# Kernel tuning notes

Measured on AMD Instinct MI355X. Metric: run time of the kernel, lower is better.

The kernel has to match this reference:

```python
import jax, jax.numpy as jnp
import numpy as np

D = 1024      # d_model
B = 16        # batch size
L = 1024      # query length
NE = 20000    # global number of entities
NB = 256      # entities per batch element (with -1 padding)
N_PAD = 32    # padded (-1) entity slots per row


def setup_inputs() -> dict:
    key = jax.random.key(0)
    ks = jax.random.split(key, 10)
    s = 1.0 / np.sqrt(D)  # torch nn.Linear default init range
    query = jax.random.normal(ks[0], (B, L, D), jnp.float32)
    ent_emb = jax.random.normal(ks[1], (NE, D), jnp.float32)
    idx = jax.random.randint(ks[2], (B, NB), 0, NE)
    idx = idx.at[:, -N_PAD:].set(-1)  # padding entities -> masked out
    WQ_w = jax.random.uniform(ks[3], (D, D), jnp.float32, -s, s)
    WQ_b = jax.random.uniform(ks[4], (D,), jnp.float32, -s, s)
    WK_w = jax.random.uniform(ks[5], (D, D), jnp.float32, -s, s)
    WK_b = jax.random.uniform(ks[6], (D,), jnp.float32, -s, s)
    WO_w = jax.random.uniform(ks[7], (D, D), jnp.float32, -s, s)
    WO_b = jax.random.uniform(ks[8], (D,), jnp.float32, -s, s)
    ln_g = jnp.ones((D,), jnp.float32)
    ln_b = jnp.zeros((D,), jnp.float32)
    return dict(query=query, ent_emb=ent_emb, ent_idx_in_batch=idx,
                max_entity_number=512,
                WQ_w=WQ_w, WQ_b=WQ_b, WK_w=WK_w, WK_b=WK_b,
                WO_w=WO_w, WO_b=WO_b, ln_g=ln_g, ln_b=ln_b)


def reference(query, ent_emb, ent_idx_in_batch, max_entity_number,
              WQ_w, WQ_b, WK_w, WK_b, WO_w, WO_b, ln_g, ln_b):
    # mask: 1.0 for real entities, 0.0 for -1 padding. (B, NB, 1)
    mask = (ent_idx_in_batch != -1).astype(query.dtype)[:, :, None]
    # gather per-batch entity embeddings (negative index wraps, then masked)
    ent_g = ent_emb[ent_idx_in_batch]                    # (B, NB, D)
    q = query @ WQ_w.T + WQ_b                            # (B, L, D)
    ent = (ent_g @ WK_w.T + WK_b) * mask                 # (B, NB, D)
    # attention scores with additive mask, then softmax
    w = jnp.einsum('byd,bnd->byn', q, ent)               # (B, L, NB)
    w = w - (1.0 - mask[:, :, 0])[:, None, :] * 100000.0
    w = jax.nn.softmax(w, axis=-1)
    # NOTE: original code uses WK (not WV) for values, and scales AFTER softmax
    d_model = query.shape[-1]
    v = jnp.einsum('byn,bnd->byd', w * (float(d_model) ** -0.5), ent)
    v = v @ WO_w.T + WO_b                                # (B, L, D)
    mu = jnp.mean(v, axis=-1, keepdims=True)
    var = jnp.var(v, axis=-1, keepdims=True)             # biased, as torch LN
    v = (v - mu) / jnp.sqrt(var + 1e-5) * ln_g + ln_b
    return v
```

## Files before the change

kernel.cpp:

```cpp
#include <hip/hip_runtime.h>
#include <hip/hip_bf16.h>
#include <cstdint>
#include <cstddef>

typedef _Float16 f16;
typedef _Float16 f16x8 __attribute__((ext_vector_type(8)));
typedef _Float16 f16x4 __attribute__((ext_vector_type(4)));
typedef float    f32x4 __attribute__((ext_vector_type(4)));

#define DM 1024
#define NBE 256

__global__ __launch_bounds__(256) void prep(
    const float* __restrict__ WO_w, f16* __restrict__ WOr,
    const float* __restrict__ WQ_w, const float* __restrict__ WK_w,
    f16* __restrict__ WQt, f16* __restrict__ WKt,
    const float* __restrict__ ent_emb, const int* __restrict__ idx,
    f16* __restrict__ Egh,
    const float* __restrict__ WQ_b, const float* __restrict__ WK_b,
    float* __restrict__ u, float* __restrict__ wobk) {
  __shared__ float ts[64][65];
  __shared__ float sm4[4];
  int blk = blockIdx.x, tid = threadIdx.x;
  if (blk < 1024) {
    int i = (blk * 256 + tid) * 4;
    float4 v = *(const float4*)(WO_w + i);
    f16x4 o; o.x = (f16)v.x; o.y = (f16)v.y; o.z = (f16)v.z; o.w = (f16)v.w;
    *(f16x4*)(WOr + i) = o;
  } else if (blk < 1536) {
    int t = blk - 1024;
    const float* in = (t >> 8) ? WK_w : WQ_w;
    f16* out = (t >> 8) ? WKt : WQt;
    int bi = ((t >> 4) & 15) * 64, bj = (t & 15) * 64;
    int tx = tid & 63, ty = tid >> 6;
#pragma unroll
    for (int k = 0; k < 16; ++k) {
      int r = ty * 16 + k;
      ts[r][tx] = in[(size_t)(bi + r) * DM + bj + tx];
    }
    __syncthreads();
#pragma unroll
    for (int k = 0; k < 16; ++k) {
      int r = ty * 16 + k;
      out[(size_t)(bj + r) * DM + bi + tx] = (f16)ts[tx][r];
    }
  } else if (blk < 5632) {
    int slot = blk - 1536;
    int e = idx[slot];
    int c = tid * 4;
    f16x4 o;
    if (e < 0) {
      o.x = (f16)0.f; o.y = (f16)0.f; o.z = (f16)0.f; o.w = (f16)0.f;
    } else {
      float4 v = *(const float4*)(ent_emb + (size_t)e * DM + c);
      o.x = (f16)v.x; o.y = (f16)v.y; o.z = (f16)v.z; o.w = (f16)v.w;
    }
    *(f16x4*)(Egh + (size_t)slot * DM + c) = o;
  } else if (blk < 5637) {
    int t = blk - 5632;
    if (t < 4) {
      int k = t * 256 + tid;
      float s = 0.f;
      for (int d = 0; d < 1024; ++d) s += WQ_b[d] * WK_w[(size_t)d * 1024 + k];
      u[k] = s;
    } else {
      float s = 0.f;
      for (int i = tid; i < 1024; i += 256) s += WK_b[i] * WQ_b[i];
#pragma unroll
      for (int d = 1; d < 64; d <<= 1) s += __shfl_xor(s, d);
      int w = tid >> 6;
      if ((tid & 63) == 0) sm4[w] = s;
      __syncthreads();
      if (tid == 0) u[1024] = sm4[0] + sm4[1] + sm4[2] + sm4[3];
    }
  } else {
    int w = tid >> 6, lane = tid & 63;
    int r = (blk - 5637) * 4 + w;
    const float* a = WO_w + (size_t)r * 1024;
    float s = 0.f;
#pragma unroll
    for (int i = 0; i < 16; ++i) s += a[lane + i * 64] * WK_b[lane + i * 64];
#pragma unroll
    for (int d = 1; d < 64; d <<= 1) s += __shfl_xor(s, d);
    if (lane == 0) wobk[r] = s;
  }
}

template <int EPI>
__device__ __forceinline__ void gemm_core(
    const f16* __restrict__ A, const f16* __restrict__ B,
    const float* __restrict__ rowbias, const int* __restrict__ colidx,
    f16* __restrict__ C, int N, int K, int m0, int n0,
    f16* __restrict__ smA, f16* __restrict__ smB) {
  int tid = threadIdx.x;
  int lane = tid & 63, w = tid >> 6;
  int wr = w >> 1, wc = w & 1;
  int l15 = lane & 15, lhi = lane >> 4;
  const f16* Ab = A + (size_t)m0 * K;
  const f16* Bb = B + (size_t)n0 * K;

  f32x4 acc[4][4];
  f32x4 z4 = {0.f, 0.f, 0.f, 0.f};
#pragma unroll
  for (int i = 0; i < 4; ++i)
#pragma unroll
    for (int j = 0; j < 4; ++j) acc[i][j] = z4;

  f16x8 ra[4], rb[4];
#pragma unroll
  for (int p = 0; p < 4; ++p) {
    int e = p * 2048 + tid * 8;
    int row = e >> 6, c8 = (e & 63) >> 3;
    ra[p] = *(const f16x8*)(Ab + (size_t)row * K + c8 * 8);
    rb[p] = *(const f16x8*)(Bb + (size_t)row * K + c8 * 8);
  }
#pragma unroll
  for (int p = 0; p < 4; ++p) {
    int e = p * 2048 + tid * 8;
    int row = e >> 6, c8 = (e & 63) >> 3;
    int off = row * 64 + ((c8 ^ (row & 7)) << 3);
    *(f16x8*)(&smA[off]) = ra[p];
    *(f16x8*)(&smB[off]) = rb[p];
  }

  int nk = K >> 6;
  for (int kt = 0; kt < nk; ++kt) {
    int cur = kt & 1;
    bool pre = (kt + 1 < nk);
    __syncthreads();
    if (pre) {
      const f16* An = Ab + (kt + 1) * 64;
      const f16* Bn = Bb + (kt + 1) * 64;
#pragma unroll
      for (int p = 0; p < 4; ++p) {
        int e = p * 2048 + tid * 8;
        int row = e >> 6, c8 = (e & 63) >> 3;
        ra[p] = *(const f16x8*)(An + (size_t)row * K + c8 * 8);
        rb[p] = *(const f16x8*)(Bn + (size_t)row * K + c8 * 8);
      }
    }
    const f16* As = smA + cur * 8192;
    const f16* Bs = smB + cur * 8192;
    __builtin_amdgcn_s_setprio(1);
#pragma unroll
    for (int kk = 0; kk < 2; ++kk) {
      int c8 = kk * 4 + lhi;
      f16x8 af[4], bf[4];
#pragma unroll
      for (int mi = 0; mi < 4; ++mi) {
        int r = wr * 64 + mi * 16 + l15;
        af[mi] = *(const f16x8*)(As + r * 64 + ((c8 ^ (r & 7)) << 3));
      }
#pragma unroll
      for (int ni = 0; ni < 4; ++ni) {
        int r = wc * 64 + ni * 16 + l15;
        bf[ni] = *(const f16x8*)(Bs + r * 64 + ((c8 ^ (r & 7)) << 3));
      }
#pragma unroll
      for (int mi = 0; mi < 4; ++mi)
#pragma unroll
        for (int ni = 0; ni < 4; ++ni)
          acc[mi][ni] = __builtin_amdgcn_mfma_f32_16x16x32_f16(af[mi], bf[ni], acc[mi][ni], 0, 0, 0);
    }
    __builtin_amdgcn_s_setprio(0);
    if (pre) {
#pragma unroll
      for (int p = 0; p < 4; ++p) {
        int e = p * 2048 + tid * 8;
        int row = e >> 6, c8 = (e & 63) >> 3;
        int off = (cur ^ 1) * 8192 + row * 64 + ((c8 ^ (row & 7)) << 3);
        *(f16x8*)(&smA[off]) = ra[p];
        *(f16x8*)(&smB[off]) = rb[p];
      }
    }
  }

#pragma unroll
  for (int mi = 0; mi < 4; ++mi) {
#pragma unroll
    for (int j = 0; j < 4; ++j) {
      int r = m0 + wr * 64 + mi * 16 + lhi * 4 + j;
      float rbv = (EPI == 3) ? rowbias[r] : 0.f;
#pragma unroll
      for (int ni = 0; ni < 4; ++ni) {
        int cN = n0 + wc * 64 + ni * 16 + l15;
        float v = acc[mi][ni][j];
        if (EPI == 3) { v += rbv; if (colidx[cN] < 0) v = 0.f; }
        C[(size_t)r * N + cN] = (f16)v;
      }
    }
  }
}

__global__ __launch_bounds__(256) void gemm_dual(const f16* __restrict__ A0,
                                                 const f16* __restrict__ A1,
                                                 const f16* __restrict__ B,
                                                 f16* __restrict__ C0,
                                                 f16* __restrict__ C1, int N, int K) {
  __shared__ __align__(16) f16 sA[2 * 8192], sB[2 * 8192];
  const f16* A = blockIdx.z ? A1 : A0;
  f16* C = blockIdx.z ? C1 : C0;
  gemm_core<0>(A, B, nullptr, nullptr, C, N, K, blockIdx.y * 128, blockIdx.x * 128, sA, sB);
}

__global__ __launch_bounds__(256) void gemm_pair(
    const f16* __restrict__ Egh, const f16* __restrict__ G, const f16* __restrict__ H,
    const float* __restrict__ wobk, const int* __restrict__ idx,
    const float* __restrict__ u,
    f16* __restrict__ Tp, f16* __restrict__ EWot, float* __restrict__ cvec) {
  __shared__ __align__(16) f16 sA[2 * 8192], sB[2 * 8192];
  int blk = blockIdx.x;
  if (blk < 256) {
    gemm_core<0>(Egh, G, nullptr, nullptr, Tp, 1024, 1024, (blk >> 3) * 128, (blk & 7) * 128, sA, sB);
  } else if (blk < 512) {
    int t = blk - 256;
    gemm_core<3>(H, Egh, wobk, idx, EWot, 4096, 1024, (t >> 5) * 128, (t & 31) * 128, sA, sB);
  } else {
    int t = blk - 512;
    int w = threadIdx.x >> 6, lane = threadIdx.x & 63;
    int n = t * 4 + w;
    const f16* e = Egh + (size_t)n * 1024;
    float s = 0.f;
#pragma unroll
    for (int i = 0; i < 16; ++i) { int k = lane + i * 64; s += (float)e[k] * u[k]; }
#pragma unroll
    for (int d = 1; d < 64; d <<= 1) s += __shfl_xor(s, d);
    if (lane == 0)
      cvec[n] = s + u[1024] + ((idx[n] < 0) ? -100000.0f : 0.0f);
  }
}

__global__ __launch_bounds__(256, 2) void attn3(
    const float* __restrict__ query, const f16* __restrict__ Tp,
    const f16* __restrict__ EWot, const float* __restrict__ cvec,
    f16* __restrict__ O16) {
  __shared__ __align__(16) char pool[49152];
  f16* smB = (f16*)pool;
  f16* smP = (f16*)(pool + 32768);
  f16* smQ = (f16*)(pool + 32768);
  __shared__ float smMax[64], smSum[64];
  int id = blockIdx.x;
  int b = id & 15, lt = id >> 4;
  int tid = threadIdx.x, lane = tid & 63, w = tid >> 6;
  int l15 = lane & 15, lhi = lane >> 4;
  int wq = w >> 1, wc = w & 1;
  const float* Qb = query + (size_t)(b * 1024 + lt * 32) * DM;
  const f16* Tb = Tp + (size_t)b * NBE * DM;

  f32x4 z4 = {0.f, 0.f, 0.f, 0.f};
  f32x4 accs[8];
#pragma unroll
  for (int i = 0; i < 8; ++i) accs[i] = z4;

  float4 rqa, rqb;
  f16x8 rb[8];
  int qrow = tid >> 3, qc0 = (tid & 7) * 8;

  rqa = *(const float4*)(Qb + (size_t)qrow * DM + qc0);
  rqb = *(const float4*)(Qb + (size_t)qrow * DM + qc0 + 4);
#pragma unroll
  for (int p = 0; p < 8; ++p) {
    int e = p * 2048 + tid * 8;
    int row = e >> 6, c8 = (e & 63) >> 3;
    rb[p] = *(const f16x8*)(Tb + (size_t)row * DM + c8 * 8);
  }

  for (int kt = 0; kt < 16; ++kt) {
    __syncthreads();
    {
      f16x8 h;
      h[0] = (f16)rqa.x; h[1] = (f16)rqa.y; h[2] = (f16)rqa.z; h[3] = (f16)rqa.w;
      h[4] = (f16)rqb.x; h[5] = (f16)rqb.y; h[6] = (f16)rqb.z; h[7] = (f16)rqb.w;
      int c8 = qc0 >> 3;
      *(f16x8*)(smQ + qrow * 64 + ((c8 ^ (qrow & 7)) << 3)) = h;
    }
#pragma unroll
    for (int p = 0; p < 8; ++p) {
      int e = p * 2048 + tid * 8;
      int row = e >> 6, c8 = (e & 63) >> 3;
      *(f16x8*)(smB + row * 64 + ((c8 ^ (row & 7)) << 3)) = rb[p];
    }
    __syncthreads();
    if (kt < 15) {
      rqa = *(const float4*)(Qb + (size_t)qrow * DM + (kt + 1) * 64 + qc0);
      rqb = *(const float4*)(Qb + (size_t)qrow * DM + (kt + 1) * 64 + qc0 + 4);
#pragma unroll
      for (int p = 0; p < 8; ++p) {
        int e = p * 2048 + tid * 8;
        int row = e >> 6, c8 = (e & 63) >> 3;
        rb[p] = *(const f16x8*)(Tb + (size_t)row * DM + (kt + 1) * 64 + c8 * 8);
      }
    }
    __builtin_amdgcn_s_setprio(1);
#pragma unroll
    for (int kk = 0; kk < 2; ++kk) {
      int c8 = kk * 4 + lhi;
      int qr = wq * 16 + l15;
      f16x8 aq = *(const f16x8*)(smQ + qr * 64 + ((c8 ^ (qr & 7)) << 3));
#pragma unroll
      for (int ni = 0; ni < 8; ++ni) {
        int er = wc * 128 + ni * 16 + l15;
        f16x8 bb = *(const f16x8*)(smB + er * 64 + ((c8 ^ (er & 7)) << 3));
        accs[ni] = __builtin_amdgcn_mfma_f32_16x16x32_f16(aq, bb, accs[ni], 0, 0, 0);
      }
    }
    __builtin_amdgcn_s_setprio(0);
  }

  const f16* Eb = EWot + (size_t)b * NBE;
#pragma unroll
  for (int p = 0; p < 8; ++p) {
    int e = p * 2048 + tid * 8;
    int row = e >> 6, c8 = (e & 63) >> 3;
    rb[p] = *(const f16x8*)(Eb + (size_t)row * 4096 + c8 * 8);
  }

  float cv[8];
#pragma unroll
  for (int ni = 0; ni < 8; ++ni)
    cv[ni] = cvec[b * NBE + wc * 128 + ni * 16 + l15];
  int rbase = wq * 16 + lhi * 4;
  float mxl[4], sml[4];
#pragma unroll
  for (int j = 0; j < 4; ++j) {
    float m = -3.0e38f;
#pragma unroll
    for (int ni = 0; ni < 8; ++ni) m = fmaxf(m, accs[ni][j] + cv[ni]);
    m = fmaxf(m, __shfl_xor(m, 1));
    m = fmaxf(m, __shfl_xor(m, 2));
    m = fmaxf(m, __shfl_xor(m, 4));
    m = fmaxf(m, __shfl_xor(m, 8));
    mxl[j] = m;
    if (l15 == 0) smMax[wc * 32 + rbase + j] = m;
  }
  __syncthreads();
#pragma unroll
  for (int j = 0; j < 4; ++j) {
    float fm = fmaxf(mxl[j], smMax[(wc ^ 1) * 32 + rbase + j]);
    float s = 0.f;
#pragma unroll
    for (int ni = 0; ni < 8; ++ni) {
      float e = __expf(accs[ni][j] + cv[ni] - fm);
      accs[ni][j] = e;
      s += e;
    }
    s += __shfl_xor(s, 1);
    s += __shfl_xor(s, 2);
    s += __shfl_xor(s, 4);
    s += __shfl_xor(s, 8);
    sml[j] = s;
    if (l15 == 0) smSum[wc * 32 + rbase + j] = s;
  }
  __syncthreads();
#pragma unroll
  for (int j = 0; j < 4; ++j) {
    float inv = 0.03125f / (sml[j] + smSum[(wc ^ 1) * 32 + rbase + j]);
    int r = rbase + j;
#pragma unroll
    for (int ni = 0; ni < 8; ++ni) {
      int col = wc * 128 + ni * 16 + l15;
      int cc8 = col >> 3;
      smP[r * 256 + ((cc8 ^ (r & 7)) << 3) + (col & 7)] = (f16)(accs[ni][j] * inv);
    }
  }

  f16* Ob = O16 + (size_t)(b * 1024 + lt * 32) * DM;
  for (int dc = 0; dc < 4; ++dc) {
    f32x4 accv[8];
#pragma unroll
    for (int i = 0; i < 8; ++i) accv[i] = z4;
    for (int ks = 0; ks < 4; ++ks) {
      __syncthreads();
#pragma unroll
      for (int p = 0; p < 8; ++p) {
        int e = p * 2048 + tid * 8;
        int row = e >> 6, c8 = (e & 63) >> 3;
        *(f16x8*)(smB + row * 64 + ((c8 ^ (row & 7)) << 3)) = rb[p];
      }
      __syncthreads();
      int nxt = dc * 4 + ks + 1;
      if (nxt < 16) {
        int ndc = nxt >> 2, nks = nxt & 3;
#pragma unroll
        for (int p = 0; p < 8; ++p) {
          int e = p * 2048 + tid * 8;
          int row = e >> 6, c8 = (e & 63) >> 3;
          rb[p] = *(const f16x8*)(Eb + (size_t)(ndc * 256 + row) * 4096 + nks * 64 + c8 * 8);
        }
      }
      __builtin_amdgcn_s_setprio(1);
#pragma unroll
      for (int kk = 0; kk < 2; ++kk) {
        int pc8 = ks * 8 + kk * 4 + lhi;
        int qr = wq * 16 + l15;
        f16x8 ap = *(const f16x8*)(smP + qr * 256 + ((pc8 ^ (qr & 7)) << 3));
        int c8 = kk * 4 + lhi;
#pragma unroll
        for (int ni = 0; ni < 8; ++ni) {
          int er = wc * 128 + ni * 16 + l15;
          f16x8 bv = *(const f16x8*)(smB + er * 64 + ((c8 ^ (er & 7)) << 3));
          accv[ni] = __builtin_amdgcn_mfma_f32_16x16x32_f16(ap, bv, accv[ni], 0, 0, 0);
        }
      }
      __builtin_amdgcn_s_setprio(0);
    }
#pragma unroll
    for (int ni = 0; ni < 8; ++ni) {
#pragma unroll
      for (int j = 0; j < 4; ++j) {
        int r = wq * 16 + lhi * 4 + j;
        int col = dc * 256 + wc * 128 + ni * 16 + l15;
        Ob[(size_t)r * DM + col] = (f16)accv[ni][j];
      }
    }
  }
}

__global__ __launch_bounds__(256) void ln_f16(const f16* __restrict__ X,
                                              const float* __restrict__ bo,
                                              const float* __restrict__ g,
                                              const float* __restrict__ bta,
                                              float* __restrict__ out) {
  size_t row = blockIdx.x;
  const f16* x = X + row * DM;
  int tid = threadIdx.x;
  f16x4 h = *(const f16x4*)(x + tid * 4);
  float4 bo4 = *(const float4*)(bo + tid * 4);
  float4 v;
  v.x = (float)h[0] + bo4.x; v.y = (float)h[1] + bo4.y;
  v.z = (float)h[2] + bo4.z; v.w = (float)h[3] + bo4.w;
  float s = v.x + v.y + v.z + v.w;
  float q = v.x * v.x + v.y * v.y + v.z * v.z + v.w * v.w;
#pragma unroll
  for (int d = 1; d < 64; d <<= 1) { s += __shfl_xor(s, d); q += __shfl_xor(q, d); }
  __shared__ float ss[4], qq[4];
  int w = tid >> 6, lane = tid & 63;
  if (lane == 0) { ss[w] = s; qq[w] = q; }
  __syncthreads();
  s = ss[0] + ss[1] + ss[2] + ss[3];
  q = qq[0] + qq[1] + qq[2] + qq[3];
  float mu = s * (1.0f / DM);
  float var = q * (1.0f / DM) - mu * mu;
  float rs = rsqrtf(var + 1e-5f);
  float4 gg = *(const float4*)(g + tid * 4);
  float4 bb = *(const float4*)(bta + tid * 4);
  float4 o;
  o.x = (v.x - mu) * rs * gg.x + bb.x;
  o.y = (v.y - mu) * rs * gg.y + bb.y;
  o.z = (v.z - mu) * rs * gg.z + bb.z;
  o.w = (v.w - mu) * rs * gg.w + bb.w;
  *(float4*)(out + row * DM + tid * 4) = o;
}

extern "C" void kernel_launch(void* const* d_in, const int* in_sizes, int n_in,
                              void* d_out, int out_size, void* d_ws, size_t ws_size,
                              hipStream_t stream) {
  const float* query   = (const float*)d_in[0];
  const float* ent_emb = (const float*)d_in[1];
  const int*   idx     = (const int*)d_in[2];
  const float* WQ_w = (const float*)d_in[4];
  const float* WQ_b = (const float*)d_in[5];
  const float* WK_w = (const float*)d_in[6];
  const float* WK_b = (const float*)d_in[7];
  const float* WO_w = (const float*)d_in[8];
  const float* WO_b = (const float*)d_in[9];
  const float* ln_g = (const float*)d_in[10];
  const float* ln_b = (const float*)d_in[11];
  float* out = (float*)d_out;

  char* p = (char*)d_ws;
  f16* Egh  = (f16*)p;  p += (size_t)4096 * 1024 * 2;
  f16* WQt  = (f16*)p;  p += (size_t)1024 * 1024 * 2;
  f16* WKt  = (f16*)p;  p += (size_t)1024 * 1024 * 2;
  f16* WOr  = (f16*)p;  p += (size_t)1024 * 1024 * 2;
  f16* G    = (f16*)p;  p += (size_t)1024 * 1024 * 2;
  f16* H    = (f16*)p;  p += (size_t)1024 * 1024 * 2;
  f16* Tp   = (f16*)p;  p += (size_t)4096 * 1024 * 2;
  f16* EWot = (f16*)p;  p += (size_t)1024 * 4096 * 2;
  f16* O16  = (f16*)p;  p += (size_t)16384 * 1024 * 2;
  float* u    = (float*)p; p += 1025 * 4;
  float* wobk = (float*)p; p += 1024 * 4;
  float* cvec = (float*)p; p += 4096 * 4;

  prep<<<5893, 256, 0, stream>>>(WO_w, WOr, WQ_w, WK_w, WQt, WKt,
                                 ent_emb, idx, Egh, WQ_b, WK_b, u, wobk);
  gemm_dual<<<dim3(8, 8, 2), 256, 0, stream>>>(WQt, WOr, WKt, G, H, 1024, 1024);
  gemm_pair<<<1536, 256, 0, stream>>>(Egh, G, H, wobk, idx, u, Tp, EWot, cvec);
  attn3<<<512, 256, 0, stream>>>(query, Tp, EWot, cvec, O16);
  ln_f16<<<16384, 256, 0, stream>>>(O16, WO_b, ln_g, ln_b, out);
}
```

Baseline: 308.0 us.

## Fuse LayerNorm into attention kernel with 64-row tiles and double-buffered LDS

The attention kernel now handles 64 query rows per block instead of 32, so 256 blocks replace 512. Q/T and EWot tiles are double-buffered in LDS, which needs one barrier per k-step instead of two, and each wave now owns a 64x64 output tile. The output bias add, row statistics and LayerNorm are fused into the kernel, which removes the separate ln_f16 launch. The f16 intermediate is still written and then re-read from global memory for the final normalization. Separately, the u-vector reduction in prep is split across 16 blocks with atomicAdd plus a memset, replacing 4 long serial loops. The larger tile and launch bound of 1 lower occupancy, and with only 256 blocks part of the GPU may sit idle.

```diff
diff --git a/kernel.cpp b/kernel.cpp
--- a/kernel.cpp
+++ b/kernel.cpp
@@ -56,26 +56,33 @@
       o.x = (f16)v.x; o.y = (f16)v.y; o.z = (f16)v.z; o.w = (f16)v.w;
     }
     *(f16x4*)(Egh + (size_t)slot * DM + c) = o;
-  } else if (blk < 5637) {
-    int t = blk - 5632;
-    if (t < 4) {
-      int k = t * 256 + tid;
-      float s = 0.f;
-      for (int d = 0; d < 1024; ++d) s += WQ_b[d] * WK_w[(size_t)d * 1024 + k];
-      u[k] = s;
-    } else {
-      float s = 0.f;
-      for (int i = tid; i < 1024; i += 256) s += WK_b[i] * WQ_b[i];
-#pragma unroll
-      for (int d = 1; d < 64; d <<= 1) s += __shfl_xor(s, d);
-      int w = tid >> 6;
-      if ((tid & 63) == 0) sm4[w] = s;
-      __syncthreads();
-      if (tid == 0) u[1024] = sm4[0] + sm4[1] + sm4[2] + sm4[3];
-    }
+  } else if (blk < 5648) {
+    int d0 = (blk - 5632) * 64;
+    float a0 = 0.f, a1 = 0.f, a2 = 0.f, a3 = 0.f;
+    for (int d = 0; d < 64; ++d) {
+      float bq = WQ_b[d0 + d];
+      const float* row = WK_w + (size_t)(d0 + d) * 1024;
+      a0 += bq * row[tid];
+      a1 += bq * row[tid + 256];
+      a2 += bq * row[tid + 512];
+      a3 += bq * row[tid + 768];
+    }
+    atomicAdd(&u[tid], a0);
+    atomicAdd(&u[tid + 256], a1);
+    atomicAdd(&u[tid + 512], a2);
+    atomicAdd(&u[tid + 768], a3);
+  } else if (blk < 5649) {
+    float s = 0.f;
+    for (int i = tid; i < 1024; i += 256) s += WK_b[i] * WQ_b[i];
+#pragma unroll
+    for (int d = 1; d < 64; d <<= 1) s += __shfl_xor(s, d);
+    int w = tid >> 6;
+    if ((tid & 63) == 0) sm4[w] = s;
+    __syncthreads();
+    if (tid == 0) u[1024] = sm4[0] + sm4[1] + sm4[2] + sm4[3];
   } else {
     int w = tid >> 6, lane = tid & 63;
-    int r = (blk - 5637) * 4 + w;
+    int r = (blk - 5649) * 4 + w;
     const float* a = WO_w + (size_t)r * 1024;
     float s = 0.f;
 #pragma unroll
@@ -230,226 +237,296 @@
   }
 }
 
-__global__ __launch_bounds__(256, 2) void attn3(
+__global__ __launch_bounds__(256, 1) void attn4(
     const float* __restrict__ query, const f16* __restrict__ Tp,
     const f16* __restrict__ EWot, const float* __restrict__ cvec,
-    f16* __restrict__ O16) {
-  __shared__ __align__(16) char pool[49152];
-  f16* smB = (f16*)pool;
-  f16* smP = (f16*)(pool + 32768);
-  f16* smQ = (f16*)(pool + 32768);
-  __shared__ float smMax[64], smSum[64];
+    const float* __restrict__ bo, const float* __restrict__ ln_g,
+    const float* __restrict__ ln_b, f16* __restrict__ O16,
+    float* __restrict__ out) {
+  __shared__ __align__(16) f16 smB[2][256 * 64];
+  __shared__ __align__(16) f16 smQ[2][64 * 64];
+  __shared__ __align__(16) f16 smP[64 * 256];
+  __shared__ float smS[256], smS2[256];
   int id = blockIdx.x;
   int b = id & 15, lt = id >> 4;
   int tid = threadIdx.x, lane = tid & 63, w = tid >> 6;
   int l15 = lane & 15, lhi = lane >> 4;
-  int wq = w >> 1, wc = w & 1;
-  const float* Qb = query + (size_t)(b * 1024 + lt * 32) * DM;
+  const float* Qb = query + (size_t)(b * 1024 + lt * 64) * DM;
   const f16* Tb = Tp + (size_t)b * NBE * DM;
+  const f16* Eb = EWot + (size_t)b * NBE;
+  size_t baserow = (size_t)(b * 1024 + lt * 64);
 
   f32x4 z4 = {0.f, 0.f, 0.f, 0.f};
-  f32x4 accs[8];
-#pragma unroll
-  for (int i = 0; i < 8; ++i) accs[i] = z4;
-
-  float4 rqa, rqb;
+  f32x4 acc[4][4];
+#pragma unroll
+  for (int i = 0; i < 4; ++i)
+#pragma unroll
+    for (int j = 0; j < 4; ++j) acc[i][j] = z4;
+
+  float4 rq[4];
   f16x8 rb[8];
-  int qrow = tid >> 3, qc0 = (tid & 7) * 8;
-
-  rqa = *(const float4*)(Qb + (size_t)qrow * DM + qc0);
-  rqb = *(const float4*)(Qb + (size_t)qrow * DM + qc0 + 4);
+  int qrow = tid >> 2, qc0 = (tid & 3) * 16;
+  int srow = tid >> 3, sc8 = tid & 7;
+
+#pragma unroll
+  for (int q = 0; q < 4; ++q) rq[q] = *(const float4*)(Qb + (size_t)qrow * DM + qc0 + q * 4);
+#pragma unroll
+  for (int p = 0; p < 8; ++p)
+    rb[p] = *(const f16x8*)(Tb + (size_t)(p * 32 + srow) * DM + sc8 * 8);
+  {
+    f16x8 h0, h1;
+    h0[0] = (f16)rq[0].x; h0[1] = (f16)rq[0].y; h0[2] = (f16)rq[0].z; h0[3] = (f16)rq[0].w;
+    h0[4] = (f16)rq[1].x; h0[5] = (f16)rq[1].y; h0[6] = (f16)rq[1].z; h0[7] = (f16)rq[1].w;
+    h1[0] = (f16)rq[2].x; h1[1] = (f16)rq[2].y; h1[2] = (f16)rq[2].z; h1[3] = (f16)rq[2].w;
+    h1[4] = (f16)rq[3].x; h1[5] = (f16)rq[3].y; h1[6] = (f16)rq[3].z; h1[7] = (f16)rq[3].w;
+    int c8a = (tid & 3) * 2;
+    *(f16x8*)(&smQ[0][qrow * 64 + ((c8a ^ (qrow & 7)) << 3)]) = h0;
+    *(f16x8*)(&smQ[0][qrow * 64 + (((c8a + 1) ^ (qrow & 7)) << 3)]) = h1;
+  }
 #pragma unroll
   for (int p = 0; p < 8; ++p) {
-    int e = p * 2048 + tid * 8;
-    int row = e >> 6, c8 = (e & 63) >> 3;
-    rb[p] = *(const f16x8*)(Tb + (size_t)row * DM + c8 * 8);
-  }
+    int row = p * 32 + srow;
+    *(f16x8*)(&smB[0][row * 64 + ((sc8 ^ (row & 7)) << 3)]) = rb[p];
+  }
+#pragma unroll
+  for (int q = 0; q < 4; ++q) rq[q] = *(const float4*)(Qb + (size_t)qrow * DM + 64 + qc0 + q * 4);
+#pragma unroll
+  for (int p = 0; p < 8; ++p)
+    rb[p] = *(const f16x8*)(Tb + (size_t)(p * 32 + srow) * DM + 64 + sc8 * 8);
+  __syncthreads();
 
   for (int kt = 0; kt < 16; ++kt) {
-    __syncthreads();
-    {
-      f16x8 h;
-      h[0] = (f16)rqa.x; h[1] = (f16)rqa.y; h[2] = (f16)rqa.z; h[3] = (f16)rqa.w;
-      h[4] = (f16)rqb.x; h[5] = (f16)rqb.y; h[6] = (f16)rqb.z; h[7] = (f16)rqb.w;
-      int c8 = qc0 >> 3;
-      *(f16x8*)(smQ + qrow * 64 + ((c8 ^ (qrow & 7)) << 3)) = h;
-    }
-#pragma unroll
-    for (int p = 0; p < 8; ++p) {
-      int e = p * 2048 + tid * 8;
-      int row = e >> 6, c8 = (e & 63) >> 3;
-      *(f16x8*)(smB + row * 64 + ((c8 ^ (row & 7)) << 3)) = rb[p];
-    }
-    __syncthreads();
+    int cur = kt & 1;
     if (kt < 15) {
-      rqa = *(const float4*)(Qb + (size_t)qrow * DM + (kt + 1) * 64 + qc0);
-      rqb = *(const float4*)(Qb + (size_t)qrow * DM + (kt + 1) * 64 + qc0 + 4);
+      f16x8 h0, h1;
+      h0[0] = (f16)rq[0].x; h0[1] = (f16)rq[0].y; h0[2] = (f16)rq[0].z; h0[3] = (f16)rq[0].w;
+      h0[4] = (f16)rq[1].x; h0[5] = (f16)rq[1].y; h0[6] = (f16)rq[1].z; h0[7] = (f16)rq[1].w;
+      h1[0] = (f16)rq[2].x; h1[1] = (f16)rq[2].y; h1[2] = (f16)rq[2].z; h1[3] = (f16)rq[2].w;
+      h1[4] = (f16)rq[3].x; h1[5] = (f16)rq[3].y; h1[6] = (f16)rq[3].z; h1[7] = (f16)rq[3].w;
+      int c8a = (tid & 3) * 2;
+      *(f16x8*)(&smQ[cur ^ 1][qrow * 64 + ((c8a ^ (qrow & 7)) << 3)]) = h0;
+      *(f16x8*)(&smQ[cur ^ 1][qrow * 64 + (((c8a + 1) ^ (qrow & 7)) << 3)]) = h1;
 #pragma unroll
       for (int p = 0; p < 8; ++p) {
-        int e = p * 2048 + tid * 8;
-        int row = e >> 6, c8 = (e & 63) >> 3;
-        rb[p] = *(const f16x8*)(Tb + (size_t)row * DM + (kt + 1) * 64 + c8 * 8);
-      }
+        int row = p * 32 + srow;
+        *(f16x8*)(&smB[cur ^ 1][row * 64 + ((sc8 ^ (row & 7)) << 3)]) = rb[p];
+      }
+    }
+    if (kt < 14) {
+#pragma unroll
+      for (int q = 0; q < 4; ++q)
+        rq[q] = *(const float4*)(Qb + (size_t)qrow * DM + (kt + 2) * 64 + qc0 + q * 4);
+#pragma unroll
+      for (int p = 0; p < 8; ++p)
+        rb[p] = *(const f16x8*)(Tb + (size_t)(p * 32 + srow) * DM + (kt + 2) * 64 + sc8 * 8);
     }
     __builtin_amdgcn_s_setprio(1);
 #pragma unroll
     for (int kk = 0; kk < 2; ++kk) {
       int c8 = kk * 4 + lhi;
-      int qr = wq * 16 + l15;
-      f16x8 aq = *(const f16x8*)(smQ + qr * 64 + ((c8 ^ (qr & 7)) << 3));
-#pragma unroll
-      for (int ni = 0; ni < 8; ++ni) {
-        int er = wc * 128 + ni * 16 + l15;
-        f16x8 bb = *(const f16x8*)(smB + er * 64 + ((c8 ^ (er & 7)) << 3));
-        accs[ni] = __builtin_amdgcn_mfma_f32_16x16x32_f16(aq, bb, accs[ni], 0, 0, 0);
-      }
+      f16x8 af[4], bf[4];
+#pragma unroll
+      for (int mi = 0; mi < 4; ++mi) {
+        int r = mi * 16 + l15;
+        af[mi] = *(const f16x8*)(&smQ[cur][r * 64 + ((c8 ^ (r & 7)) << 3)]);
+      }
+#pragma unroll
+      for (int ni = 0; ni < 4; ++ni) {
+        int er = w * 64 + ni * 16 + l15;
+        bf[ni] = *(const f16x8*)(&smB[cur][er * 64 + ((c8 ^ (er & 7)) << 3)]);
+      }
+#pragma unroll
+      for (int mi = 0; mi < 4; ++mi)
+#pragma unroll
+        for (int ni = 0; ni < 4; ++ni)
+          acc[mi][ni] = __builtin_amdgcn_mfma_f32_16x16x32_f16(af[mi], bf[ni], acc[mi][ni], 0, 0, 0);
     }
     __builtin_amdgcn_s_setprio(0);
-  }
-
-  const f16* Eb = EWot + (size_t)b * NBE;
+    __syncthreads();
+  }
+
+#pragma unroll
+  for (int p = 0; p < 8; ++p)
+    rb[p] = *(const f16x8*)(Eb + (size_t)(p * 32 + srow) * 4096 + sc8 * 8);
+
+  float cv[4];
+#pragma unroll
+  for (int ni = 0; ni < 4; ++ni)
+    cv[ni] = cvec[b * NBE + w * 64 + ni * 16 + l15];
+#pragma unroll
+  for (int mi = 0; mi < 4; ++mi)
+#pragma unroll
+    for (int j = 0; j < 4; ++j) {
+      float m = -3.0e38f;
+#pragma unroll
+      for (int ni = 0; ni < 4; ++ni) m = fmaxf(m, acc[mi][ni][j] + cv[ni]);
+      m = fmaxf(m, __shfl_xor(m, 1));
+      m = fmaxf(m, __shfl_xor(m, 2));
+      m = fmaxf(m, __shfl_xor(m, 4));
+      m = fmaxf(m, __shfl_xor(m, 8));
+      if (l15 == 0) smS[w * 64 + mi * 16 + lhi * 4 + j] = m;
+    }
+  __syncthreads();
+#pragma unroll
+  for (int mi = 0; mi < 4; ++mi)
+#pragma unroll
+    for (int j = 0; j < 4; ++j) {
+      int r = mi * 16 + lhi * 4 + j;
+      float fm = fmaxf(fmaxf(smS[r], smS[64 + r]), fmaxf(smS[128 + r], smS[192 + r]));
+      float s = 0.f;
+#pragma unroll
+      for (int ni = 0; ni < 4; ++ni) {
+        float e = __expf(acc[mi][ni][j] + cv[ni] - fm);
+        acc[mi][ni][j] = e;
+        s += e;
+      }
+      s += __shfl_xor(s, 1);
+      s += __shfl_xor(s, 2);
+      s += __shfl_xor(s, 4);
+      s += __shfl_xor(s, 8);
+      if (l15 == 0) smS2[w * 64 + r] = s;
+    }
+  __syncthreads();
+#pragma unroll
+  for (int mi = 0; mi < 4; ++mi)
+#pragma unroll
+    for (int j = 0; j < 4; ++j) {
+      int r = mi * 16 + lhi * 4 + j;
+      float inv = 0.03125f / (smS2[r] + smS2[64 + r] + smS2[128 + r] + smS2[192 + r]);
+#pragma unroll
+      for (int ni = 0; ni < 4; ++ni) {
+        int col = w * 64 + ni * 16 + l15;
+        int cc8 = col >> 3;
+        smP[r * 256 + ((cc8 ^ (r & 7)) << 3) + (col & 7)] = (f16)(acc[mi][ni][j] * inv);
+      }
+    }
+
 #pragma unroll
   for (int p = 0; p < 8; ++p) {
-    int e = p * 2048 + tid * 8;
-    int row = e >> 6, c8 = (e & 63) >> 3;
-    rb[p] = *(const f16x8*)(Eb + (size_t)row * 4096 + c8 * 8);
-  }
-
-  float cv[8];
-#pragma unroll
-  for (int ni = 0; ni < 8; ++ni)
-    cv[ni] = cvec[b * NBE + wc * 128 + ni * 16 + l15];
-  int rbase = wq * 16 + lhi * 4;
-  float mxl[4], sml[4];
-#pragma unroll
-  for (int j = 0; j < 4; ++j) {
-    float m = -3.0e38f;
-#pragma unroll
-    for (int ni = 0; ni < 8; ++ni) m = fmaxf(m, accs[ni][j] + cv[ni]);
-    m = fmaxf(m, __shfl_xor(m, 1));
-    m = fmaxf(m, __shfl_xor(m, 2));
-    m = fmaxf(m, __shfl_xor(m, 4));
-    m = fmaxf(m, __shfl_xor(m, 8));
-    mxl[j] = m;
-    if (l15 == 0) smMax[wc * 32 + rbase + j] = m;
+    int row = p * 32 + srow;
+    *(f16x8*)(&smB[0][row * 64 + ((sc8 ^ (row & 7)) << 3)]) = rb[p];
   }
   __syncthreads();
 #pragma unroll
-  for (int j = 0; j < 4; ++j) {
-    float fm = fmaxf(mxl[j], smMax[(wc ^ 1) * 32 + rbase + j]);
-    float s = 0.f;
-#pragma unroll
-    for (int ni = 0; ni < 8; ++ni) {
-      float e = __expf(accs[ni][j] + cv[ni] - fm);
-      accs[ni][j] = e;
-      s += e;
-    }
-    s += __shfl_xor(s, 1);
-    s += __shfl_xor(s, 2);
-    s += __shfl_xor(s, 4);
-    s += __shfl_xor(s, 8);
-    sml[j] = s;
-    if (l15 == 0) smSum[wc * 32 + rbase + j] = s;
-  }
+  for (int p = 0; p < 8; ++p)
+    rb[p] = *(const f16x8*)(Eb + (size_t)(p * 32 + srow) * 4096 + 64 + sc8 * 8);
+
+  float sum_[4][4], sq_[4][4];
+#pragma unroll
+  for (int mi = 0; mi < 4; ++mi)
+#pragma unroll
+    for (int j = 0; j < 4; ++j) { sum_[mi][j] = 0.f; sq_[mi][j] = 0.f; }
+  f32x4 accv[4][4];
+
+  for (int t = 0; t < 16; ++t) {
+    int cur = t & 1;
+    if ((t & 3) == 0) {
+#pragma unroll
+      for (int i = 0; i < 4; ++i)
+#pragma unroll
+        for (int j = 0; j < 4; ++j) accv[i][j] = z4;
+    }
+    if (t < 15) {
+#pragma unroll
+      for (int p = 0; p < 8; ++p) {
+        int row = p * 32 + srow;
+        *(f16x8*)(&smB[cur ^ 1][row * 64 + ((sc8 ^ (row & 7)) << 3)]) = rb[p];
+      }
+    }
+    if (t < 14) {
+      int nt = t + 2;
+#pragma unroll
+      for (int p = 0; p < 8; ++p)
+        rb[p] = *(const f16x8*)(Eb + (size_t)((nt >> 2) * 256 + p * 32 + srow) * 4096 + (nt & 3) * 64 + sc8 * 8);
+    }
+    __builtin_amdgcn_s_setprio(1);
+#pragma unroll
+    for (int kk = 0; kk < 2; ++kk) {
+      int pc8 = (t & 3) * 8 + kk * 4 + lhi;
+      int c8 = kk * 4 + lhi;
+      f16x8 ap[4], bf[4];
+#pragma unroll
+      for (int mi = 0; mi < 4; ++mi) {
+        int qr = mi * 16 + l15;
+        ap[mi] = *(const f16x8*)(&smP[qr * 256 + ((pc8 ^ (qr & 7)) << 3)]);
+      }
+#pragma unroll
+      for (int ni = 0; ni < 4; ++ni) {
+        int er = w * 64 + ni * 16 + l15;
+        bf[ni] = *(const f16x8*)(&smB[cur][er * 64 + ((c8 ^ (er & 7)) << 3)]);
+      }
+#pragma unroll
+      for (int mi = 0; mi < 4; ++mi)
+#pragma unroll
+        for (int ni = 0; ni < 4; ++ni)
+          accv[mi][ni] = __builtin_amdgcn_mfma_f32_16x16x32_f16(ap[mi], bf[ni], accv[mi][ni], 0, 0, 0);
+    }
+    __builtin_amdgcn_s_setprio(0);
+    if ((t & 3) == 3) {
+      int dc = t >> 2;
+#pragma unroll
+      for (int ni = 0; ni < 4; ++ni) {
+        int col = dc * 256 + w * 64 + ni * 16 + l15;
+        float bov = bo[col];
+#pragma unroll
+        for (int mi = 0; mi < 4; ++mi)
+#pragma unroll
+          for (int j = 0; j < 4; ++j) {
+            float v = accv[mi][ni][j] + bov;
+            int r = mi * 16 + lhi * 4 + j;
+            O16[(baserow + r) * DM + col] = (f16)v;
+            sum_[mi][j] += v;
+            sq_[mi][j] += v * v;
+          }
+      }
+    }
+    __syncthreads();
+  }
+
+  asm volatile("s_waitcnt vmcnt(0)" ::: "memory");
+#pragma unroll
+  for (int mi = 0; mi < 4; ++mi)
+#pragma unroll
+    for (int j = 0; j < 4; ++j) {
+      float s = sum_[mi][j], q = sq_[mi][j];
+      s += __shfl_xor(s, 1); q += __shfl_xor(q, 1);
+      s += __shfl_xor(s, 2); q += __shfl_xor(q, 2);
+      s += __shfl_xor(s, 4); q += __shfl_xor(q, 4);
+      s += __shfl_xor(s, 8); q += __shfl_xor(q, 8);
+      if (l15 == 0) {
+        smS[w * 64 + mi * 16 + lhi * 4 + j] = s;
+        smS2[w * 64 + mi * 16 + lhi * 4 + j] = q;
+      }
+    }
   __syncthreads();
-#pragma unroll
-  for (int j = 0; j < 4; ++j) {
-    float inv = 0.03125f / (sml[j] + smSum[(wc ^ 1) * 32 + rbase + j]);
-    int r = rbase + j;
-#pragma unroll
-    for (int ni = 0; ni < 8; ++ni) {
-      int col = wc * 128 + ni * 16 + l15;
-      int cc8 = col >> 3;
-      smP[r * 256 + ((cc8 ^ (r & 7)) << 3) + (col & 7)] = (f16)(accs[ni][j] * inv);
-    }
-  }
-
-  f16* Ob = O16 + (size_t)(b * 1024 + lt * 32) * DM;
-  for (int dc = 0; dc < 4; ++dc) {
-    f32x4 accv[8];
-#pragma unroll
-    for (int i = 0; i < 8; ++i) accv[i] = z4;
-    for (int ks = 0; ks < 4; ++ks) {
-      __syncthreads();
-#pragma unroll
-      for (int p = 0; p < 8; ++p) {
-        int e = p * 2048 + tid * 8;
-        int row = e >> 6, c8 = (e & 63) >> 3;
-        *(f16x8*)(smB + row * 64 + ((c8 ^ (row & 7)) << 3)) = rb[p];
-      }
-      __syncthreads();
-      int nxt = dc * 4 + ks + 1;
-      if (nxt < 16) {
-        int ndc = nxt >> 2, nks = nxt & 3;
-#pragma unroll
-        for (int p = 0; p < 8; ++p) {
-          int e = p * 2048 + tid * 8;
-          int row = e >> 6, c8 = (e & 63) >> 3;
-          rb[p] = *(const f16x8*)(Eb + (size_t)(ndc * 256 + row) * 4096 + nks * 64 + c8 * 8);
+  float gv[4][4], bv[4][4];
+#pragma unroll
+  for (int dc = 0; dc < 4; ++dc)
+#pragma unroll
+    for (int ni = 0; ni < 4; ++ni) {
+      int col = dc * 256 + w * 64 + ni * 16 + l15;
+      gv[dc][ni] = ln_g[col];
+      bv[dc][ni] = ln_b[col];
+    }
+#pragma unroll
+  for (int mi = 0; mi < 4; ++mi)
+#pragma unroll
+    for (int j = 0; j < 4; ++j) {
+      int r = mi * 16 + lhi * 4 + j;
+      float S = smS[r] + smS[64 + r] + smS[128 + r] + smS[192 + r];
+      float Q2 = smS2[r] + smS2[64 + r] + smS2[128 + r] + smS2[192 + r];
+      float mu = S * (1.0f / DM);
+      float var = Q2 * (1.0f / DM) - mu * mu;
+      float rs = rsqrtf(var + 1e-5f);
+#pragma unroll
+      for (int dc = 0; dc < 4; ++dc)
+#pragma unroll
+        for (int ni = 0; ni < 4; ++ni) {
+          int col = dc * 256 + w * 64 + ni * 16 + l15;
+          float h = (float)O16[(baserow + r) * DM + col];
+          out[(baserow + r) * DM + col] = (h - mu) * rs * gv[dc][ni] + bv[dc][ni];
         }
-      }
-      __builtin_amdgcn_s_setprio(1);
-#pragma unroll
-      for (int kk = 0; kk < 2; ++kk) {
-        int pc8 = ks * 8 + kk * 4 + lhi;
-        int qr = wq * 16 + l15;
-        f16x8 ap = *(const f16x8*)(smP + qr * 256 + ((pc8 ^ (qr & 7)) << 3));
-        int c8 = kk * 4 + lhi;
-#pragma unroll
-        for (int ni = 0; ni < 8; ++ni) {
-          int er = wc * 128 + ni * 16 + l15;
-          f16x8 bv = *(const f16x8*)(smB + er * 64 + ((c8 ^ (er & 7)) << 3));
-          accv[ni] = __builtin_amdgcn_mfma_f32_16x16x32_f16(ap, bv, accv[ni], 0, 0, 0);
-        }
-      }
-      __builtin_amdgcn_s_setprio(0);
-    }
-#pragma unroll
-    for (int ni = 0; ni < 8; ++ni) {
-#pragma unroll
-      for (int j = 0; j < 4; ++j) {
-        int r = wq * 16 + lhi * 4 + j;
-        int col = dc * 256 + wc * 128 + ni * 16 + l15;
-        Ob[(size_t)r * DM + col] = (f16)accv[ni][j];
-      }
-    }
-  }
-}
-
-__global__ __launch_bounds__(256) void ln_f16(const f16* __restrict__ X,
-                                              const float* __restrict__ bo,
-                                              const float* __restrict__ g,
-                                              const float* __restrict__ bta,
-                                              float* __restrict__ out) {
-  size_t row = blockIdx.x;
-  const f16* x = X + row * DM;
-  int tid = threadIdx.x;
-  f16x4 h = *(const f16x4*)(x + tid * 4);
-  float4 bo4 = *(const float4*)(bo + tid * 4);
-  float4 v;
-  v.x = (float)h[0] + bo4.x; v.y = (float)h[1] + bo4.y;
-  v.z = (float)h[2] + bo4.z; v.w = (float)h[3] + bo4.w;
-  float s = v.x + v.y + v.z + v.w;
-  float q = v.x * v.x + v.y * v.y + v.z * v.z + v.w * v.w;
-#pragma unroll
-  for (int d = 1; d < 64; d <<= 1) { s += __shfl_xor(s, d); q += __shfl_xor(q, d); }
-  __shared__ float ss[4], qq[4];
-  int w = tid >> 6, lane = tid & 63;
-  if (lane == 0) { ss[w] = s; qq[w] = q; }
-  __syncthreads();
-  s = ss[0] + ss[1] + ss[2] + ss[3];
-  q = qq[0] + qq[1] + qq[2] + qq[3];
-  float mu = s * (1.0f / DM);
-  float var = q * (1.0f / DM) - mu * mu;
-  float rs = rsqrtf(var + 1e-5f);
-  float4 gg = *(const float4*)(g + tid * 4);
-  float4 bb = *(const float4*)(bta + tid * 4);
-  float4 o;
-  o.x = (v.x - mu) * rs * gg.x + bb.x;
-  o.y = (v.y - mu) * rs * gg.y + bb.y;
-  o.z = (v.z - mu) * rs * gg.z + bb.z;
-  o.w = (v.w - mu) * rs * gg.w + bb.w;
-  *(float4*)(out + row * DM + tid * 4) = o;
+    }
 }
 
 extern "C" void kernel_launch(void* const* d_in, const int* in_sizes, int n_in,
@@ -482,10 +559,10 @@
   float* wobk = (float*)p; p += 1024 * 4;
   float* cvec = (float*)p; p += 4096 * 4;
 
-  prep<<<5893, 256, 0, stream>>>(WO_w, WOr, WQ_w, WK_w, WQt, WKt,
+  hipMemsetAsync(u, 0, 1025 * sizeof(float), stream);
+  prep<<<5905, 256, 0, stream>>>(WO_w, WOr, WQ_w, WK_w, WQt, WKt,
                                  ent_emb, idx, Egh, WQ_b, WK_b, u, wobk);
   gemm_dual<<<dim3(8, 8, 2), 256, 0, stream>>>(WQt, WOr, WKt, G, H, 1024, 1024);
   gemm_pair<<<1536, 256, 0, stream>>>(Egh, G, H, wobk, idx, u, Tp, EWot, cvec);
-  attn3<<<512, 256, 0, stream>>>(query, Tp, EWot, cvec, O16);
-  ln_f16<<<16384, 256, 0, stream>>>(O16, WO_b, ln_g, ln_b, out);
+  attn4<<<256, 256, 0, stream>>>(query, Tp, EWot, cvec, WO_b, ln_g, ln_b, O16, out);
 }
```

After: 288.8 us. 1.07x faster.
